# Kernel optimization log

Measured on AMD Instinct MI355X. Metric: run time of the kernel, lower is better.

Reference implementation:

```python
import jax, jax.numpy as jnp
import numpy as np

L = 43          # number of classes
C = L + 3       # <eps>, 'O', 'I-', + L class symbols
B = 128
T = 4096
NEG = jnp.float32(-1e30)


def setup_inputs() -> dict:
    key = jax.random.key(0)
    k1, k2, k3, k4 = jax.random.split(key, 4)
    logits = jax.random.normal(k1, (B, T, C), dtype=jnp.float32)
    log_probs = jax.nn.log_softmax(logits, axis=-1)
    input_lens = jax.random.randint(k2, (B,), T // 2, T + 1).astype(jnp.int32)
    labels = jax.random.randint(k3, (B, T), 1, C).astype(jnp.int32)  # valid (non-eps) symbols
    # den_scores parameter: one raw score per denominator arc (2L+4 arcs).
    # Layout: [0]=0->0 'O', [1:L+1]=0->0 labels, [L+1]=0->1 'I-', [L+2]=0->final,
    #         [L+3]=1->1 'I-', [L+4:2L+4]=1->0 labels.
    den_params = 0.01 * jax.random.normal(k4, (2 * L + 4,), dtype=jnp.float32)
    return {"log_probs": log_probs, "den_params": den_params,
            "input_lens": input_lens, "labels": labels}


def reference(log_probs, den_params, input_lens, labels):
    Bb, Tt, Cc = log_probs.shape
    Ll = Cc - 3
    # set_scores_stochastic_: per-source-state log-softmax of arc scores
    g0 = jax.nn.log_softmax(den_params[: Ll + 3])   # state-0 outgoing arcs
    g1 = jax.nn.log_softmax(den_params[Ll + 3:])    # state-1 outgoing arcs
    s_O, s0_lab, s_0I, s_fin = g0[0], g0[1:Ll + 1], g0[Ll + 1], g0[Ll + 2]
    s_1I, s1_lab = g1[0], g1[1:]

    mask = jnp.arange(Tt)[None, :] < input_lens[:, None]          # [B,T]

    # ---- numerator: linear FSA intersected with emissions = path score ----
    tok_lp = jnp.take_along_axis(log_probs, labels[..., None], axis=-1)[..., 0]
    num = jnp.sum(jnp.where(mask, tok_lp, 0.0), axis=1)           # [B]

    # ---- denominator: log-semiring forward DP over the 2-state topology ----
    lp_t = jnp.moveaxis(log_probs, 1, 0)    # [T,B,C]
    mask_t = jnp.moveaxis(mask, 1, 0)       # [T,B]

    def step(alpha, inputs):
        lp, m = inputs                       # lp [B,C], m [B]
        a0, a1 = alpha[:, 0], alpha[:, 1]
        lp_lab = lp[:, 3:]                   # emissions for class symbols, [B,L]
        # into state 0: 0->0 on 'O', 0->0 on each label, 1->0 on each label
        terms0 = jnp.concatenate([
            (a0 + s_O + lp[:, 1])[:, None],
            a0[:, None] + s0_lab[None, :] + lp_lab,
            a1[:, None] + s1_lab[None, :] + lp_lab,
        ], axis=1)
        n0 = jax.scipy.special.logsumexp(terms0, axis=1)
        # into state 1: 0->1 and 1->1, both on 'I-'
        terms1 = jnp.stack([a0 + s_0I + lp[:, 2], a1 + s_1I + lp[:, 2]], axis=1)
        n1 = jax.scipy.special.logsumexp(terms1, axis=1)
        new = jnp.stack([n0, n1], axis=1)
        new = jnp.where(m[:, None], new, alpha)  # frozen past each seq's length
        return new, None

    alpha0 = jnp.concatenate(
        [jnp.zeros((Bb, 1), log_probs.dtype), jnp.full((Bb, 1), NEG, log_probs.dtype)], axis=1)
    alpha, _ = jax.lax.scan(step, alpha0, (lp_t, mask_t))
    den = alpha[:, 0] + s_fin                                    # final arc 0->2 on -1

    return jnp.sum(num - den)
```

## Files before the change

kernel.cpp:

```cpp
#include <hip/hip_runtime.h>

#define BB 128
#define TT 4096
#define LL 43
#define CC 46
#define CHUNK 64
#define NC (TT / CHUNK)
#define NEGF (-1e30f)
#define L2E 1.44269504088896340736f
#define LN2 0.69314718055994530942f

__device__ __forceinline__ float fexp2(float x) { return __builtin_amdgcn_exp2f(x); }
__device__ __forceinline__ float flog2(float x) { return __builtin_amdgcn_logf(x); }
__device__ __forceinline__ float frcp(float x)  { return __builtin_amdgcn_rcpf(x); }

__global__ __launch_bounds__(64) void crf_chunk(
    const float* __restrict__ lp, const float* __restrict__ dp,
    const int* __restrict__ lens, const int* __restrict__ labels,
    float* __restrict__ res, float* __restrict__ out) {
    __shared__ float tile[CHUNK * CC];
    __shared__ float2 pp[LL + 1];
    __shared__ float sc[4];

    int b = blockIdx.y, c = blockIdx.x;
    int t0 = c * CHUNK;
    int len = lens[b];
    int lane = threadIdx.x;
    float* r = res + (b * NC + c) * 8;

    if (b == 0 && c == 0 && lane == 0) out[0] = 0.f;

    if (t0 >= len) {
        if (lane == 0) {
            *(float4*)r = make_float4(0.f, NEGF, NEGF, 0.f);
            r[4] = 0.f;
        }
        return;
    }

    {
        const float* gsrc = lp + (size_t)(b * TT + t0) * CC;
        #pragma unroll
        for (int s = 0; s < 11; ++s) {
            const float* g = gsrc + s * 256 + lane * 4;
            float* l = tile + s * 256;
            __builtin_amdgcn_global_load_lds(
                (const __attribute__((address_space(1))) void*)g,
                (__attribute__((address_space(3))) void*)l, 16, 0, 0);
        }
        if (lane < 32) {
            const float* g = gsrc + 11 * 256 + lane * 4;
            float* l = tile + 11 * 256;
            __builtin_amdgcn_global_load_lds(
                (const __attribute__((address_space(1))) void*)g,
                (__attribute__((address_space(3))) void*)l, 16, 0, 0);
        }
    }

    {
        float x0 = (lane < CC) ? dp[lane] : NEGF;
        float x1 = (lane < LL + 1) ? dp[CC + lane] : NEGF;
        float e0 = fexp2(L2E * x0);
        float e1 = fexp2(L2E * x1);
        float s0 = e0, s1 = e1;
        #pragma unroll
        for (int m = 1; m < 64; m <<= 1) {
            s0 += __shfl_xor(s0, m);
            s1 += __shfl_xor(s1, m);
        }
        float r0 = frcp(s0), r1 = frcp(s1);
        float g0 = L2E * x0 - flog2(s0);
        float g1 = L2E * x1 - flog2(s1);
        if (lane >= 1 && lane <= LL) { pp[lane - 1].x = e0 * r0; pp[lane - 1].y = e1 * r1; }
        if (lane == 0) { sc[0] = e0 * r0; sc[2] = g1; }
        if (lane == LL + 1) sc[1] = g0;
    }

    int t = t0 + lane;
    int lab = labels[b * TT + t];
    __syncthreads();

    const float* vr = tile + lane * CC;
    float m00, m01, m10, m11, tok;
    {
        const float2* vr2 = (const float2*)vr;
        float2 c01 = vr2[0];
        float2 c23 = vr2[1];
        tok = vr[lab];
        float w1 = fexp2(L2E * c01.y);
        float v2s = L2E * c23.x;
        float dot0 = sc[0] * w1;
        float dot1 = 0.f;
        {
            float w = fexp2(L2E * c23.y);
            float2 p = pp[0];
            dot0 = fmaf(p.x, w, dot0);
            dot1 = fmaf(p.y, w, dot1);
        }
        #pragma unroll
        for (int k = 2; k <= 22; ++k) {
            float2 v = vr2[k];
            float wa = fexp2(L2E * v.x), wb = fexp2(L2E * v.y);
            float2 pa = pp[2 * k - 3], pb = pp[2 * k - 2];
            dot0 = fmaf(pa.x, wa, dot0); dot1 = fmaf(pa.y, wa, dot1);
            dot0 = fmaf(pb.x, wb, dot0); dot1 = fmaf(pb.y, wb, dot1);
        }
        m00 = dot0;
        m01 = dot1;
        m10 = fexp2(sc[1] + v2s);
        m11 = fexp2(sc[2] + v2s);
    }
    int ie = 0;
    if (t >= len) { m00 = 1.f; m01 = 0.f; m10 = 0.f; m11 = 1.f; tok = 0.f; }

    #pragma unroll
    for (int lev = 0; lev < 6; ++lev) {
        int m = 1 << lev;
        float p00 = __shfl_xor(m00, m), p01 = __shfl_xor(m01, m);
        float p10 = __shfl_xor(m10, m), p11 = __shfl_xor(m11, m);
        int   pe  = __shfl_xor(ie, m);
        float ptk = __shfl_xor(tok, m);
        bool up = (lane & m) != 0;
        float a00 = up ? m00 : p00, a01 = up ? m01 : p01;
        float a10 = up ? m10 : p10, a11 = up ? m11 : p11;
        float b00 = up ? p00 : m00, b01 = up ? p01 : m01;
        float b10 = up ? p10 : m10, b11 = up ? p11 : m11;
        float n00 = fmaf(a01, b10, a00 * b00);
        float n01 = fmaf(a01, b11, a00 * b01);
        float n10 = fmaf(a11, b10, a10 * b00);
        float n11 = fmaf(a11, b11, a10 * b01);
        ie += pe;
        tok += ptk;
        if (lev & 1) {
            float mx = fmaxf(fmaxf(n00, n01), fmaxf(n10, n11));
            unsigned bi = __float_as_uint(mx) >> 23;
            float scl = __uint_as_float((254u - bi) << 23);
            n00 *= scl; n01 *= scl; n10 *= scl; n11 *= scl;
            ie += (int)bi - 127;
        }
        m00 = n00; m01 = n01; m10 = n10; m11 = n11;
    }
    if (lane == 0) {
        float fe = (float)ie;
        float4 v = make_float4(flog2(m00) + fe, flog2(m01) + fe,
                               flog2(m10) + fe, flog2(m11) + fe);
        *(float4*)r = v;
        r[4] = tok;
    }
}

__global__ __launch_bounds__(256) void crf_final(
    const float* __restrict__ dp, const float* __restrict__ res,
    float* __restrict__ out) {
    int wv = threadIdx.x >> 6, lane = threadIdx.x & 63;
    int b = blockIdx.x * 4 + wv;

    float sfin2;
    {
        float x0 = (lane < CC) ? dp[lane] : NEGF;
        float e0 = fexp2(L2E * x0);
        float s0 = e0;
        #pragma unroll
        for (int m = 1; m < 64; m <<= 1) s0 += __shfl_xor(s0, m);
        float g0 = L2E * x0 - flog2(s0);
        sfin2 = __shfl(g0, LL + 2);
    }

    const float* r = res + (b * NC + lane) * 8;
    float4 rv = *(const float4*)r;
    float tok = r[4];
    float rm = fmaxf(fmaxf(rv.x, rv.y), fmaxf(rv.z, rv.w));
    int ie = (int)__builtin_floorf(rm);
    float fe = (float)ie;
    float m00 = fexp2(rv.x - fe), m01 = fexp2(rv.y - fe);
    float m10 = fexp2(rv.z - fe), m11 = fexp2(rv.w - fe);

    #pragma unroll
    for (int m = 1; m < 64; m <<= 1) {
        float p00 = __shfl_xor(m00, m), p01 = __shfl_xor(m01, m);
        float p10 = __shfl_xor(m10, m), p11 = __shfl_xor(m11, m);
        int   pe  = __shfl_xor(ie, m);
        float ptk = __shfl_xor(tok, m);
        bool up = (lane & m) != 0;
        float a00 = up ? m00 : p00, a01 = up ? m01 : p01;
        float a10 = up ? m10 : p10, a11 = up ? m11 : p11;
        float b00 = up ? p00 : m00, b01 = up ? p01 : m01;
        float b10 = up ? p10 : m10, b11 = up ? p11 : m11;
        float n00 = fmaf(a01, b10, a00 * b00);
        float n01 = fmaf(a01, b11, a00 * b01);
        float n10 = fmaf(a11, b10, a10 * b00);
        float n11 = fmaf(a11, b11, a10 * b01);
        float mx = fmaxf(fmaxf(n00, n01), fmaxf(n10, n11));
        unsigned bi = __float_as_uint(mx) >> 23;
        float scl = __uint_as_float((254u - bi) << 23);
        m00 = n00 * scl; m01 = n01 * scl;
        m10 = n10 * scl; m11 = n11 * scl;
        ie = ie + pe + (int)bi - 127;
        tok += ptk;
    }
    if (lane == 0) {
        float den2 = flog2(m00) + (float)ie + sfin2;
        float val = tok - den2 * LN2;
        atomicAdd(out, val);
    }
}

extern "C" void kernel_launch(void* const* d_in, const int* in_sizes, int n_in,
                              void* d_out, int out_size, void* d_ws, size_t ws_size,
                              hipStream_t stream) {
    const float* lp = (const float*)d_in[0];
    const float* dp = (const float*)d_in[1];
    const int* lens = (const int*)d_in[2];
    const int* labels = (const int*)d_in[3];
    float* out = (float*)d_out;
    float* res = (float*)d_ws;

    hipLaunchKernelGGL(crf_chunk, dim3(NC, BB), dim3(64), 0, stream,
                       lp, dp, lens, labels, res, out);
    hipLaunchKernelGGL(crf_final, dim3(BB / 4), dim3(256), 0, stream, dp, res, out);
}
```

Before: 148.4 us.

## Fuse chunk scan and final reduction via last-block atomic counters

Merges the per-chunk scan kernel and the final per-batch combine kernel into one launch. Each block bumps a per-batch atomic counter, and the last block for a batch does the cross-chunk combine. A global counter then lets the last batch sum all batch values deterministically. This removes one kernel launch and its gap, but adds a memset, atomic traffic and fences, and the result writes now depend on acq_rel ordering of the results buffer.

```diff
diff --git a/kernel.cpp b/kernel.cpp
--- a/kernel.cpp
+++ b/kernel.cpp
@@ -14,10 +14,11 @@
 __device__ __forceinline__ float flog2(float x) { return __builtin_amdgcn_logf(x); }
 __device__ __forceinline__ float frcp(float x)  { return __builtin_amdgcn_rcpf(x); }
 
-__global__ __launch_bounds__(64) void crf_chunk(
+__global__ __launch_bounds__(64) void crf_fused(
     const float* __restrict__ lp, const float* __restrict__ dp,
     const int* __restrict__ lens, const int* __restrict__ labels,
-    float* __restrict__ res, float* __restrict__ out) {
+    float* __restrict__ res, float* __restrict__ val,
+    int* __restrict__ cnt, float* __restrict__ out) {
     __shared__ float tile[CHUNK * CC];
     __shared__ float2 pp[LL + 1];
     __shared__ float sc[4];
@@ -28,180 +29,192 @@
     int lane = threadIdx.x;
     float* r = res + (b * NC + c) * 8;
 
-    if (b == 0 && c == 0 && lane == 0) out[0] = 0.f;
-
     if (t0 >= len) {
         if (lane == 0) {
             *(float4*)r = make_float4(0.f, NEGF, NEGF, 0.f);
             r[4] = 0.f;
         }
-        return;
+    } else {
+        {
+            const float* gsrc = lp + (size_t)(b * TT + t0) * CC;
+            #pragma unroll
+            for (int s = 0; s < 11; ++s) {
+                const float* g = gsrc + s * 256 + lane * 4;
+                float* l = tile + s * 256;
+                __builtin_amdgcn_global_load_lds(
+                    (const __attribute__((address_space(1))) void*)g,
+                    (__attribute__((address_space(3))) void*)l, 16, 0, 0);
+            }
+            if (lane < 32) {
+                const float* g = gsrc + 11 * 256 + lane * 4;
+                float* l = tile + 11 * 256;
+                __builtin_amdgcn_global_load_lds(
+                    (const __attribute__((address_space(1))) void*)g,
+                    (__attribute__((address_space(3))) void*)l, 16, 0, 0);
+            }
+        }
+
+        {
+            float x0 = (lane < CC) ? dp[lane] : NEGF;
+            float x1 = (lane < LL + 1) ? dp[CC + lane] : NEGF;
+            float e0 = fexp2(L2E * x0);
+            float e1 = fexp2(L2E * x1);
+            float s0 = e0, s1 = e1;
+            #pragma unroll
+            for (int m = 1; m < 64; m <<= 1) {
+                s0 += __shfl_xor(s0, m);
+                s1 += __shfl_xor(s1, m);
+            }
+            float r0 = frcp(s0), r1 = frcp(s1);
+            float g0 = L2E * x0 - flog2(s0);
+            float g1 = L2E * x1 - flog2(s1);
+            if (lane >= 1 && lane <= LL) { pp[lane - 1].x = e0 * r0; pp[lane - 1].y = e1 * r1; }
+            if (lane == 0) { sc[0] = e0 * r0; sc[2] = g1; }
+            if (lane == LL + 1) sc[1] = g0;
+        }
+
+        int t = t0 + lane;
+        int lab = labels[b * TT + t];
+        __syncthreads();
+
+        const float* vr = tile + lane * CC;
+        float m00, m01, m10, m11, tok;
+        {
+            const float2* vr2 = (const float2*)vr;
+            float2 c01 = vr2[0];
+            float2 c23 = vr2[1];
+            tok = vr[lab];
+            float w1 = fexp2(L2E * c01.y);
+            float v2s = L2E * c23.x;
+            float dot0 = sc[0] * w1;
+            float dot1 = 0.f;
+            {
+                float w = fexp2(L2E * c23.y);
+                float2 p = pp[0];
+                dot0 = fmaf(p.x, w, dot0);
+                dot1 = fmaf(p.y, w, dot1);
+            }
+            #pragma unroll
+            for (int k = 2; k <= 22; ++k) {
+                float2 v = vr2[k];
+                float wa = fexp2(L2E * v.x), wb = fexp2(L2E * v.y);
+                float2 pa = pp[2 * k - 3], pb = pp[2 * k - 2];
+                dot0 = fmaf(pa.x, wa, dot0); dot1 = fmaf(pa.y, wa, dot1);
+                dot0 = fmaf(pb.x, wb, dot0); dot1 = fmaf(pb.y, wb, dot1);
+            }
+            m00 = dot0;
+            m01 = dot1;
+            m10 = fexp2(sc[1] + v2s);
+            m11 = fexp2(sc[2] + v2s);
+        }
+        int ie = 0;
+        if (t >= len) { m00 = 1.f; m01 = 0.f; m10 = 0.f; m11 = 1.f; tok = 0.f; }
+
+        #pragma unroll
+        for (int lev = 0; lev < 6; ++lev) {
+            int m = 1 << lev;
+            float p00 = __shfl_xor(m00, m), p01 = __shfl_xor(m01, m);
+            float p10 = __shfl_xor(m10, m), p11 = __shfl_xor(m11, m);
+            int   pe  = __shfl_xor(ie, m);
+            float ptk = __shfl_xor(tok, m);
+            bool up = (lane & m) != 0;
+            float a00 = up ? m00 : p00, a01 = up ? m01 : p01;
+            float a10 = up ? m10 : p10, a11 = up ? m11 : p11;
+            float b00 = up ? p00 : m00, b01 = up ? p01 : m01;
+            float b10 = up ? p10 : m10, b11 = up ? p11 : m11;
+            float n00 = fmaf(a01, b10, a00 * b00);
+            float n01 = fmaf(a01, b11, a00 * b01);
+            float n10 = fmaf(a11, b10, a10 * b00);
+            float n11 = fmaf(a11, b11, a10 * b01);
+            ie += pe;
+            tok += ptk;
+            if (lev & 1) {
+                float mx = fmaxf(fmaxf(n00, n01), fmaxf(n10, n11));
+                unsigned bi = __float_as_uint(mx) >> 23;
+                float scl = __uint_as_float((254u - bi) << 23);
+                n00 *= scl; n01 *= scl; n10 *= scl; n11 *= scl;
+                ie += (int)bi - 127;
+            }
+            m00 = n00; m01 = n01; m10 = n10; m11 = n11;
+        }
+        if (lane == 0) {
+            float fe = (float)ie;
+            float4 v = make_float4(flog2(m00) + fe, flog2(m01) + fe,
+                                   flog2(m10) + fe, flog2(m11) + fe);
+            *(float4*)r = v;
+            r[4] = tok;
+        }
     }
 
-    {
-        const float* gsrc = lp + (size_t)(b * TT + t0) * CC;
-        #pragma unroll
-        for (int s = 0; s < 11; ++s) {
-            const float* g = gsrc + s * 256 + lane * 4;
-            float* l = tile + s * 256;
-            __builtin_amdgcn_global_load_lds(
-                (const __attribute__((address_space(1))) void*)g,
-                (__attribute__((address_space(3))) void*)l, 16, 0, 0);
-        }
-        if (lane < 32) {
-            const float* g = gsrc + 11 * 256 + lane * 4;
-            float* l = tile + 11 * 256;
-            __builtin_amdgcn_global_load_lds(
-                (const __attribute__((address_space(1))) void*)g,
-                (__attribute__((address_space(3))) void*)l, 16, 0, 0);
-        }
-    }
-
-    {
-        float x0 = (lane < CC) ? dp[lane] : NEGF;
-        float x1 = (lane < LL + 1) ? dp[CC + lane] : NEGF;
-        float e0 = fexp2(L2E * x0);
-        float e1 = fexp2(L2E * x1);
-        float s0 = e0, s1 = e1;
+    int old = 0;
+    if (lane == 0)
+        old = __hip_atomic_fetch_add(&cnt[b], 1, __ATOMIC_ACQ_REL,
+                                     __HIP_MEMORY_SCOPE_AGENT);
+    old = __shfl(old, 0);
+    if (old == NC - 1) {
+        __threadfence();
+
+        float sfin2;
+        {
+            float x0 = (lane < CC) ? dp[lane] : NEGF;
+            float e0 = fexp2(L2E * x0);
+            float s0 = e0;
+            #pragma unroll
+            for (int m = 1; m < 64; m <<= 1) s0 += __shfl_xor(s0, m);
+            float g0 = L2E * x0 - flog2(s0);
+            sfin2 = __shfl(g0, LL + 2);
+        }
+
+        const float* rr = res + (b * NC + lane) * 8;
+        float4 rv = *(const float4*)rr;
+        float tk = rr[4];
+        float rm = fmaxf(fmaxf(rv.x, rv.y), fmaxf(rv.z, rv.w));
+        int ie = (int)__builtin_floorf(rm);
+        float fe = (float)ie;
+        float m00 = fexp2(rv.x - fe), m01 = fexp2(rv.y - fe);
+        float m10 = fexp2(rv.z - fe), m11 = fexp2(rv.w - fe);
+
         #pragma unroll
         for (int m = 1; m < 64; m <<= 1) {
-            s0 += __shfl_xor(s0, m);
-            s1 += __shfl_xor(s1, m);
-        }
-        float r0 = frcp(s0), r1 = frcp(s1);
-        float g0 = L2E * x0 - flog2(s0);
-        float g1 = L2E * x1 - flog2(s1);
-        if (lane >= 1 && lane <= LL) { pp[lane - 1].x = e0 * r0; pp[lane - 1].y = e1 * r1; }
-        if (lane == 0) { sc[0] = e0 * r0; sc[2] = g1; }
-        if (lane == LL + 1) sc[1] = g0;
-    }
-
-    int t = t0 + lane;
-    int lab = labels[b * TT + t];
-    __syncthreads();
-
-    const float* vr = tile + lane * CC;
-    float m00, m01, m10, m11, tok;
-    {
-        const float2* vr2 = (const float2*)vr;
-        float2 c01 = vr2[0];
-        float2 c23 = vr2[1];
-        tok = vr[lab];
-        float w1 = fexp2(L2E * c01.y);
-        float v2s = L2E * c23.x;
-        float dot0 = sc[0] * w1;
-        float dot1 = 0.f;
-        {
-            float w = fexp2(L2E * c23.y);
-            float2 p = pp[0];
-            dot0 = fmaf(p.x, w, dot0);
-            dot1 = fmaf(p.y, w, dot1);
-        }
-        #pragma unroll
-        for (int k = 2; k <= 22; ++k) {
-            float2 v = vr2[k];
-            float wa = fexp2(L2E * v.x), wb = fexp2(L2E * v.y);
-            float2 pa = pp[2 * k - 3], pb = pp[2 * k - 2];
-            dot0 = fmaf(pa.x, wa, dot0); dot1 = fmaf(pa.y, wa, dot1);
-            dot0 = fmaf(pb.x, wb, dot0); dot1 = fmaf(pb.y, wb, dot1);
-        }
-        m00 = dot0;
-        m01 = dot1;
-        m10 = fexp2(sc[1] + v2s);
-        m11 = fexp2(sc[2] + v2s);
-    }
-    int ie = 0;
-    if (t >= len) { m00 = 1.f; m01 = 0.f; m10 = 0.f; m11 = 1.f; tok = 0.f; }
-
-    #pragma unroll
-    for (int lev = 0; lev < 6; ++lev) {
-        int m = 1 << lev;
-        float p00 = __shfl_xor(m00, m), p01 = __shfl_xor(m01, m);
-        float p10 = __shfl_xor(m10, m), p11 = __shfl_xor(m11, m);
-        int   pe  = __shfl_xor(ie, m);
-        float ptk = __shfl_xor(tok, m);
-        bool up = (lane & m) != 0;
-        float a00 = up ? m00 : p00, a01 = up ? m01 : p01;
-        float a10 = up ? m10 : p10, a11 = up ? m11 : p11;
-        float b00 = up ? p00 : m00, b01 = up ? p01 : m01;
-        float b10 = up ? p10 : m10, b11 = up ? p11 : m11;
-        float n00 = fmaf(a01, b10, a00 * b00);
-        float n01 = fmaf(a01, b11, a00 * b01);
-        float n10 = fmaf(a11, b10, a10 * b00);
-        float n11 = fmaf(a11, b11, a10 * b01);
-        ie += pe;
-        tok += ptk;
-        if (lev & 1) {
+            float p00 = __shfl_xor(m00, m), p01 = __shfl_xor(m01, m);
+            float p10 = __shfl_xor(m10, m), p11 = __shfl_xor(m11, m);
+            int   pe  = __shfl_xor(ie, m);
+            float ptk = __shfl_xor(tk, m);
+            bool up = (lane & m) != 0;
+            float a00 = up ? m00 : p00, a01 = up ? m01 : p01;
+            float a10 = up ? m10 : p10, a11 = up ? m11 : p11;
+            float b00 = up ? p00 : m00, b01 = up ? p01 : m01;
+            float b10 = up ? p10 : m10, b11 = up ? p11 : m11;
+            float n00 = fmaf(a01, b10, a00 * b00);
+            float n01 = fmaf(a01, b11, a00 * b01);
+            float n10 = fmaf(a11, b10, a10 * b00);
+            float n11 = fmaf(a11, b11, a10 * b01);
             float mx = fmaxf(fmaxf(n00, n01), fmaxf(n10, n11));
             unsigned bi = __float_as_uint(mx) >> 23;
             float scl = __uint_as_float((254u - bi) << 23);
-            n00 *= scl; n01 *= scl; n10 *= scl; n11 *= scl;
-            ie += (int)bi - 127;
-        }
-        m00 = n00; m01 = n01; m10 = n10; m11 = n11;
-    }
-    if (lane == 0) {
-        float fe = (float)ie;
-        float4 v = make_float4(flog2(m00) + fe, flog2(m01) + fe,
-                               flog2(m10) + fe, flog2(m11) + fe);
-        *(float4*)r = v;
-        r[4] = tok;
-    }
-}
-
-__global__ __launch_bounds__(256) void crf_final(
-    const float* __restrict__ dp, const float* __restrict__ res,
-    float* __restrict__ out) {
-    int wv = threadIdx.x >> 6, lane = threadIdx.x & 63;
-    int b = blockIdx.x * 4 + wv;
-
-    float sfin2;
-    {
-        float x0 = (lane < CC) ? dp[lane] : NEGF;
-        float e0 = fexp2(L2E * x0);
-        float s0 = e0;
-        #pragma unroll
-        for (int m = 1; m < 64; m <<= 1) s0 += __shfl_xor(s0, m);
-        float g0 = L2E * x0 - flog2(s0);
-        sfin2 = __shfl(g0, LL + 2);
-    }
-
-    const float* r = res + (b * NC + lane) * 8;
-    float4 rv = *(const float4*)r;
-    float tok = r[4];
-    float rm = fmaxf(fmaxf(rv.x, rv.y), fmaxf(rv.z, rv.w));
-    int ie = (int)__builtin_floorf(rm);
-    float fe = (float)ie;
-    float m00 = fexp2(rv.x - fe), m01 = fexp2(rv.y - fe);
-    float m10 = fexp2(rv.z - fe), m11 = fexp2(rv.w - fe);
-
-    #pragma unroll
-    for (int m = 1; m < 64; m <<= 1) {
-        float p00 = __shfl_xor(m00, m), p01 = __shfl_xor(m01, m);
-        float p10 = __shfl_xor(m10, m), p11 = __shfl_xor(m11, m);
-        int   pe  = __shfl_xor(ie, m);
-        float ptk = __shfl_xor(tok, m);
-        bool up = (lane & m) != 0;
-        float a00 = up ? m00 : p00, a01 = up ? m01 : p01;
-        float a10 = up ? m10 : p10, a11 = up ? m11 : p11;
-        float b00 = up ? p00 : m00, b01 = up ? p01 : m01;
-        float b10 = up ? p10 : m10, b11 = up ? p11 : m11;
-        float n00 = fmaf(a01, b10, a00 * b00);
-        float n01 = fmaf(a01, b11, a00 * b01);
-        float n10 = fmaf(a11, b10, a10 * b00);
-        float n11 = fmaf(a11, b11, a10 * b01);
-        float mx = fmaxf(fmaxf(n00, n01), fmaxf(n10, n11));
-        unsigned bi = __float_as_uint(mx) >> 23;
-        float scl = __uint_as_float((254u - bi) << 23);
-        m00 = n00 * scl; m01 = n01 * scl;
-        m10 = n10 * scl; m11 = n11 * scl;
-        ie = ie + pe + (int)bi - 127;
-        tok += ptk;
-    }
-    if (lane == 0) {
-        float den2 = flog2(m00) + (float)ie + sfin2;
-        float val = tok - den2 * LN2;
-        atomicAdd(out, val);
+            m00 = n00 * scl; m01 = n01 * scl;
+            m10 = n10 * scl; m11 = n11 * scl;
+            ie = ie + pe + (int)bi - 127;
+            tk += ptk;
+        }
+
+        if (lane == 0) {
+            float den2 = flog2(m00) + (float)ie + sfin2;
+            val[b] = tk - den2 * LN2;
+        }
+
+        int g = 0;
+        if (lane == 0)
+            g = __hip_atomic_fetch_add(&cnt[BB], 1, __ATOMIC_ACQ_REL,
+                                       __HIP_MEMORY_SCOPE_AGENT);
+        g = __shfl(g, 0);
+        if (g == BB - 1) {
+            __threadfence();
+            float v = val[lane] + val[lane + 64];
+            #pragma unroll
+            for (int m = 1; m < 64; m <<= 1) v += __shfl_xor(v, m);
+            if (lane == 0) out[0] = v;
+        }
     }
 }
 
@@ -214,8 +227,10 @@
     const int* labels = (const int*)d_in[3];
     float* out = (float*)d_out;
     float* res = (float*)d_ws;
-
-    hipLaunchKernelGGL(crf_chunk, dim3(NC, BB), dim3(64), 0, stream,
-                       lp, dp, lens, labels, res, out);
-    hipLaunchKernelGGL(crf_final, dim3(BB / 4), dim3(256), 0, stream, dp, res, out);
+    float* val = res + BB * NC * 8;
+    int* cnt = (int*)(val + BB);
+
+    hipMemsetAsync(cnt, 0, (BB + 1) * sizeof(int), stream);
+    hipLaunchKernelGGL(crf_fused, dim3(NC, BB), dim3(64), 0, stream,
+                       lp, dp, lens, labels, res, val, cnt, out);
 }
```

Result: slower. 458.1 us (+208.7%).
